# Performance work log

Measured on AMD Instinct MI355X. Metric: run time of the kernel, lower is better.

## Reference

```python
import jax, jax.numpy as jnp
import numpy as np

C = 256
HEADS = 4
GROUPS = 8
EPS = 1e-5


def setup_inputs() -> dict:
    key = jax.random.key(0)
    ks = jax.random.split(key, 7)
    B, H, W = 2, 64, 64
    x = jax.random.normal(ks[0], (B, C, H, W), dtype=jnp.float32)
    gamma = jnp.ones((C,), dtype=jnp.float32)
    beta = jnp.zeros((C,), dtype=jnp.float32)
    # conv 1x1 weights stored as [out_ch, in_ch]
    w_qkv = jax.random.normal(ks[1], (3 * C, C), dtype=jnp.float32) * (1.0 / np.sqrt(C))
    b_qkv = jax.random.normal(ks[2], (3 * C,), dtype=jnp.float32) * 0.01
    w_proj = jax.random.normal(ks[3], (C, C), dtype=jnp.float32) * (1.0 / np.sqrt(C))
    b_proj = jax.random.normal(ks[4], (C,), dtype=jnp.float32) * 0.01
    return {"x": x, "gamma": gamma, "beta": beta, "w_qkv": w_qkv,
            "b_qkv": b_qkv, "w_proj": w_proj, "b_proj": b_proj}


def _group_norm(x, gamma, beta):
    B, Cc, H, W = x.shape
    xg = x.reshape(B, GROUPS, Cc // GROUPS, H, W)
    mean = xg.mean(axis=(2, 3, 4), keepdims=True)
    var = xg.var(axis=(2, 3, 4), keepdims=True)
    xg = (xg - mean) * jax.lax.rsqrt(var + EPS)
    xn = xg.reshape(B, Cc, H, W)
    return xn * gamma[None, :, None, None] + beta[None, :, None, None]


def reference(x, gamma, beta, w_qkv, b_qkv, w_proj, b_proj):
    B, Cc, H, W = x.shape
    N = H * W
    hd = Cc // HEADS
    residual = x
    xn = _group_norm(x, gamma, beta)
    # 1x1 conv == channel matmul: [B,3C,H,W]
    qkv = jnp.einsum('oc,bchw->bohw', w_qkv, xn) + b_qkv[None, :, None, None]
    # [B,3,heads,hd,N] -> (3,B,heads,N,hd)
    qkv = qkv.reshape(B, 3, HEADS, hd, N).transpose(1, 0, 2, 4, 3)
    q, k, v = qkv[0], qkv[1], qkv[2]
    scale = hd ** -0.5
    attn = jax.nn.softmax(jnp.einsum('bhnd,bhmd->bhnm', q, k) * scale, axis=-1)
    out = jnp.einsum('bhnm,bhmd->bhnd', attn, v)  # [B,heads,N,hd]
    out = out.transpose(0, 1, 3, 2).reshape(B, Cc, H, W)
    out = jnp.einsum('oc,bchw->bohw', w_proj, out) + b_proj[None, :, None, None]
    return out + residual
```

## Files before the change

### kernel.cpp

```cpp
#include <hip/hip_runtime.h>
#include <stdint.h>

#define EPS 1e-5f

typedef float f32x4 __attribute__((ext_vector_type(4)));
typedef float f32x16 __attribute__((ext_vector_type(16)));
typedef __bf16 bf16x8 __attribute__((ext_vector_type(8)));
typedef uint32_t u32x4 __attribute__((ext_vector_type(4)));

__device__ __forceinline__ ushort f2bf(float f){
  union { float f; uint32_t u; } v; v.f = f;
  uint32_t r = v.u + 0x7fffu + ((v.u >> 16) & 1u);
  return (ushort)(r >> 16);
}

__device__ __forceinline__ float bf2f(ushort u){
  union { uint32_t u; float f; } v; v.u = ((uint32_t)u) << 16;
  return v.f;
}

__device__ __forceinline__ uint32_t pk2bf(float a, float b){
  __bf16 x = (__bf16)a, y = (__bf16)b;
  return (uint32_t)__builtin_bit_cast(ushort, x) |
         ((uint32_t)__builtin_bit_cast(ushort, y) << 16);
}

__device__ __forceinline__ f32x4 mfma16(bf16x8 a, bf16x8 b, f32x4 c){
  return __builtin_amdgcn_mfma_f32_16x16x32_bf16(a, b, c, 0, 0, 0);
}
__device__ __forceinline__ f32x16 mfma32(bf16x8 a, bf16x8 b, f32x16 c){
  return __builtin_amdgcn_mfma_f32_32x32x16_bf16(a, b, c, 0, 0, 0);
}

__global__ __launch_bounds__(256) void k_pg(const float* wq, const float* wp, const float* x,
                                            ushort* wqb, ushort* wpb, float2* part){
  __shared__ float red[8];
  int bid = blockIdx.x;
  if (bid < 768){
    int i = bid * 256 + threadIdx.x;
    if (i < 3*256*256) wqb[i] = f2bf(wq[i]);
    if (i < 256*256)   wpb[i] = f2bf(wp[i]);
    return;
  }
  int gb = bid - 768;
  int bg = gb >> 6, pb = gb & 63;
  const f32x4* base = (const f32x4*)(x + (size_t)bg*131072 + (size_t)pb*2048);
  float s = 0.f, ss = 0.f;
  #pragma unroll
  for (int it = 0; it < 2; ++it){
    f32x4 v = base[threadIdx.x + it*256];
    #pragma unroll
    for (int j = 0; j < 4; ++j){ s += v[j]; ss += v[j]*v[j]; }
  }
  #pragma unroll
  for (int off = 1; off < 64; off <<= 1){
    s  += __shfl_xor(s,  off);
    ss += __shfl_xor(ss, off);
  }
  int wid = threadIdx.x >> 6;
  if ((threadIdx.x & 63) == 0){ red[wid] = s; red[4 + wid] = ss; }
  __syncthreads();
  if (threadIdx.x == 0){
    part[gb] = make_float2(red[0]+red[1]+red[2]+red[3],
                           red[4]+red[5]+red[6]+red[7]);
  }
}

__global__ __launch_bounds__(512) void k_nqkv(const float* x, const float* gamma, const float* beta,
                                              const float2* part, const ushort* wqb, const float* bqkv,
                                              ushort* Qf, ushort* Kf, ushort* Vf){
  __shared__ ushort A[32][264];
  __shared__ ushort Cl[32][136];
  __shared__ ushort Cl_T[128][40];
  __shared__ float2 st[8];
  int nt = blockIdx.x, b = blockIdx.y;
  int t = threadIdx.x, lane = t & 63, wid = t >> 6;

  {
    float2 p = part[(b*8 + wid)*64 + lane];
    float s = p.x, ss = p.y;
    #pragma unroll
    for (int off = 1; off < 64; off <<= 1){
      s  += __shfl_xor(s,  off);
      ss += __shfl_xor(ss, off);
    }
    if (lane == 0){
      const float inv = 1.f / 131072.f;
      float mean = s * inv;
      float var  = ss * inv - mean*mean;
      st[wid] = make_float2(mean, rsqrtf(var + EPS));
    }
  }
  __syncthreads();

  {
    int c = t >> 1, nh = t & 1;
    float2 s0 = st[c >> 5];
    float g  = gamma[c] * s0.y;
    float bt = beta[c] - s0.x * g;
    const float* xr = x + ((size_t)(b*256 + c))*4096 + nt*32 + nh*16;
    #pragma unroll
    for (int j4 = 0; j4 < 4; ++j4){
      f32x4 v = *(const f32x4*)(xr + j4*4);
      #pragma unroll
      for (int e = 0; e < 4; ++e) A[nh*16 + j4*4 + e][c] = f2bf(v[e]*g + bt);
    }
  }
  __syncthreads();

  int l15 = lane & 15, g4 = lane >> 4;
  f32x4 acc[6][2];
  #pragma unroll
  for (int of = 0; of < 6; ++of)
    #pragma unroll
    for (int mf = 0; mf < 2; ++mf) acc[of][mf] = (f32x4){0.f,0.f,0.f,0.f};

  #pragma unroll
  for (int ks = 0; ks < 8; ++ks){
    bf16x8 a0 = *(const bf16x8*)&A[l15][ks*32 + g4*8];
    bf16x8 a1 = *(const bf16x8*)&A[16 + l15][ks*32 + g4*8];
    #pragma unroll
    for (int of = 0; of < 6; ++of){
      int o = of*128 + wid*16 + l15;
      bf16x8 bw = *(const bf16x8*)(wqb + (size_t)o*256 + ks*32 + g4*8);
      acc[of][0] = mfma16(a0, bw, acc[of][0]);
      acc[of][1] = mfma16(a1, bw, acc[of][1]);
    }
  }

  #pragma unroll
  for (int of = 0; of < 6; ++of){
    __syncthreads();
    float bias = bqkv[of*128 + wid*16 + l15];
    if (of < 4){
      #pragma unroll
      for (int mf = 0; mf < 2; ++mf)
        #pragma unroll
        for (int r = 0; r < 4; ++r)
          Cl[mf*16 + g4*4 + r][wid*16 + l15] = f2bf(acc[of][mf][r] + bias);
    } else {
      #pragma unroll
      for (int mf = 0; mf < 2; ++mf)
        *(uint2*)&Cl_T[wid*16 + l15][mf*16 + g4*4] =
          make_uint2(pk2bf(acc[of][mf][0]+bias, acc[of][mf][1]+bias),
                     pk2bf(acc[of][mf][2]+bias, acc[of][mf][3]+bias));
    }
    __syncthreads();

    int hp = t >> 8;
    int hh = (of & 1)*2 + hp;
    if (of < 4){
      int rem = t & 255, dsub = rem >> 6, ln = rem & 63, h2 = ln >> 5, p31 = ln & 31;
      int row = (of < 2) ? p31 : ((p31 & 19) | ((p31 & 4) << 1) | ((p31 & 8) >> 1));
      ushort* basep = (of < 2) ? Qf : Kf;
      uint4 v = *(const uint4*)&Cl[row][hp*64 + dsub*16 + h2*8];
      *(uint4*)(basep + ((size_t)(b*4 + hh))*262144 + nt*2048 + dsub*512 + ln*8) = v;
    } else {
      int rem = t & 255, dt = rem >> 7, r2 = rem & 127, c4h = r2 >> 5, p31 = r2 & 31;
      int c4 = (nt & 1)*2 + (c4h >> 1), h2 = c4h & 1;
      int n0 = (c4h >> 1)*16 + h2*8;
      int ln = h2*32 + p31;
      uint4 v = *(const uint4*)&Cl_T[hp*64 + dt*32 + p31][n0];
      *(uint4*)(Vf + ((size_t)(b*4 + hh))*262144 + (size_t)(nt >> 1)*4096
                   + dt*2048 + c4*512 + ln*8) = v;
    }
  }
}

template<int SPLIT>
__global__ __launch_bounds__(64, 3) void k_attn(const ushort* Qf, const ushort* Kf,
                                                const ushort* Vf, ushort* Opart, float2* ML){
  const float SCL2 = 0.125f * 1.44269504f;
  int bh = blockIdx.x & 7;
  int within = blockIdx.x >> 3;
  int sp = within >> 7, qt = within & 127;
  int l = threadIdx.x, l31 = l & 31, hi = l >> 5;

  const ushort* Qg = Qf + (size_t)bh*262144 + qt*2048 + l*8;
  const ushort* Kg = Kf + (size_t)bh*262144 + l*8;
  const ushort* Vg = Vf + (size_t)bh*262144 + l*8;

  bf16x8 qf[4];
  #pragma unroll
  for (int dsub = 0; dsub < 4; ++dsub)
    qf[dsub] = *(const bf16x8*)(Qg + dsub*512);

  f32x16 o[2];
  #pragma unroll
  for (int dt = 0; dt < 2; ++dt)
    #pragma unroll
    for (int r = 0; r < 16; ++r) o[dt][r] = 0.f;
  float m_s = -INFINITY, l_s = 0.f;

  const int kbBeg = sp * (64 / SPLIT), kbEnd = kbBeg + 64 / SPLIT;
  for (int kb = kbBeg; kb < kbEnd; ++kb){
    bf16x8 kf[2][4];
    #pragma unroll
    for (int kt = 0; kt < 2; ++kt)
      #pragma unroll
      for (int dsub = 0; dsub < 4; ++dsub)
        kf[kt][dsub] = *(const bf16x8*)(Kg + (size_t)(kb*2 + kt)*2048 + dsub*512);

    bf16x8 vf[2][4];
    #pragma unroll
    for (int dt = 0; dt < 2; ++dt)
      #pragma unroll
      for (int c4 = 0; c4 < 4; ++c4)
        vf[dt][c4] = *(const bf16x8*)(Vg + (size_t)kb*4096 + dt*2048 + c4*512);

    f32x16 s[2];
    __builtin_amdgcn_s_setprio(1);
    #pragma unroll
    for (int kt = 0; kt < 2; ++kt){
      f32x16 acc;
      #pragma unroll
      for (int r = 0; r < 16; ++r) acc[r] = 0.f;
      #pragma unroll
      for (int dsub = 0; dsub < 4; ++dsub)
        acc = mfma32(kf[kt][dsub], qf[dsub], acc);
      s[kt] = acc;
    }
    __builtin_amdgcn_s_setprio(0);

    f32x16 mx = s[0];
    #pragma unroll
    for (int r = 0; r < 16; ++r) mx[r] = fmaxf(mx[r], s[1][r]);
    #pragma unroll
    for (int off = 8; off > 0; off >>= 1)
      #pragma unroll
      for (int r = 0; r < off; ++r) mx[r] = fmaxf(mx[r], mx[r + off]);
    float vm = fmaxf(mx[0], __shfl_xor(mx[0], 32)) * SCL2;

    if (__any(vm > m_s + 8.f)){
      float mn = fmaxf(m_s, vm);
      float a = __builtin_amdgcn_exp2f(m_s - mn);
      m_s = mn; l_s *= a;
      #pragma unroll
      for (int dt = 0; dt < 2; ++dt)
        #pragma unroll
        for (int r = 0; r < 16; ++r) o[dt][r] *= a;
    }
    {
      float r0 = 0.f, r1 = 0.f, r2 = 0.f, r3 = 0.f;
      #pragma unroll
      for (int kt = 0; kt < 2; ++kt)
        #pragma unroll
        for (int r = 0; r < 16; r += 4){
          float e0 = __builtin_amdgcn_exp2f(__builtin_fmaf(s[kt][r+0], SCL2, -m_s));
          float e1 = __builtin_amdgcn_exp2f(__builtin_fmaf(s[kt][r+1], SCL2, -m_s));
          float e2 = __builtin_amdgcn_exp2f(__builtin_fmaf(s[kt][r+2], SCL2, -m_s));
          float e3 = __builtin_amdgcn_exp2f(__builtin_fmaf(s[kt][r+3], SCL2, -m_s));
          s[kt][r+0] = e0; s[kt][r+1] = e1;
          s[kt][r+2] = e2; s[kt][r+3] = e3;
          r0 += e0; r1 += e1; r2 += e2; r3 += e3;
        }
      float rr = (r0 + r1) + (r2 + r3);
      rr += __shfl_xor(rr, 32);
      l_s += rr;
    }

    bf16x8 pf[2][2];
    #pragma unroll
    for (int kt = 0; kt < 2; ++kt)
      #pragma unroll
      for (int ks = 0; ks < 2; ++ks){
        u32x4 w;
        #pragma unroll
        for (int c = 0; c < 4; ++c)
          w[c] = pk2bf(s[kt][8*ks + 2*c], s[kt][8*ks + 2*c + 1]);
        pf[kt][ks] = __builtin_bit_cast(bf16x8, w);
      }

    __builtin_amdgcn_s_setprio(1);
    #pragma unroll
    for (int dt = 0; dt < 2; ++dt)
      #pragma unroll
      for (int kt = 0; kt < 2; ++kt)
        #pragma unroll
        for (int ks = 0; ks < 2; ++ks)
          o[dt] = mfma32(vf[dt][kt*2 + ks], pf[kt][ks], o[dt]);
    __builtin_amdgcn_s_setprio(0);
  }

  int pw = (bh*SPLIT + sp)*128 + qt;
  if (hi == 0) ML[(size_t)pw*32 + l31] = make_float2(m_s, l_s);
  ushort* dst = Opart + (size_t)pw*2048;
  #pragma unroll
  for (int dt = 0; dt < 2; ++dt)
    #pragma unroll
    for (int rq = 0; rq < 4; ++rq){
      int d0 = dt*32 + rq*8 + 4*hi;
      uint2 w = make_uint2(pk2bf(o[dt][rq*4+0], o[dt][rq*4+1]),
                           pk2bf(o[dt][rq*4+2], o[dt][rq*4+3]));
      *(uint2*)(dst + (size_t)l31*64 + d0) = w;
    }
}

template<int SPLIT>
__global__ __launch_bounds__(512) void k_cproj(const ushort* Opart, const float2* ML,
                                               const ushort* wpb, const float* bproj,
                                               const float* x, float* out){
  __shared__ ushort A[64][264];
  int nt = blockIdx.x, b = blockIdx.y;
  int t = threadIdx.x;

  int n_local = t >> 3, d0 = (t & 7) * 8;
  int tile = n_local >> 5, ql = n_local & 31;
  int qt32 = nt*2 + tile;
  #pragma unroll
  for (int h = 0; h < 4; ++h){
    int bh = b*4 + h;
    float2 mls[SPLIT];
    float m = -INFINITY;
    #pragma unroll
    for (int sp = 0; sp < SPLIT; ++sp){
      mls[sp] = ML[((size_t)((bh*SPLIT + sp)*128 + qt32))*32 + ql];
      m = fmaxf(m, mls[sp].x);
    }
    float den = 0.f, w[SPLIT];
    #pragma unroll
    for (int sp = 0; sp < SPLIT; ++sp){
      w[sp] = __builtin_amdgcn_exp2f(mls[sp].x - m);
      den += mls[sp].y * w[sp];
    }
    float inv = 1.f / den;
    float vals[8];
    #pragma unroll
    for (int j = 0; j < 8; ++j) vals[j] = 0.f;
    #pragma unroll
    for (int sp = 0; sp < SPLIT; ++sp){
      const ushort* src = Opart + ((size_t)((bh*SPLIT + sp)*128 + qt32))*2048 + (size_t)ql*64 + d0;
      uint4 a0 = *(const uint4*)src;
      float f = w[sp] * inv;
      #pragma unroll
      for (int j = 0; j < 8; ++j) vals[j] += bf2f(((const ushort*)&a0)[j]) * f;
    }
    uint32_t pk[4];
    #pragma unroll
    for (int j = 0; j < 4; ++j) pk[j] = pk2bf(vals[2*j], vals[2*j+1]);
    *(uint4*)&A[n_local][h*64 + d0] = make_uint4(pk[0], pk[1], pk[2], pk[3]);
  }
  __syncthreads();

  int lane = t & 63, wid = t >> 6, l15 = lane & 15, g4 = lane >> 4;
  f32x4 acc[4][2];
  #pragma unroll
  for (int mf = 0; mf < 4; ++mf)
    #pragma unroll
    for (int of = 0; of < 2; ++of) acc[mf][of] = (f32x4){0.f,0.f,0.f,0.f};

  #pragma unroll
  for (int ks = 0; ks < 8; ++ks){
    bf16x8 aa[4];
    #pragma unroll
    for (int mf = 0; mf < 4; ++mf)
      aa[mf] = *(const bf16x8*)&A[mf*16 + l15][ks*32 + g4*8];
    #pragma unroll
    for (int of = 0; of < 2; ++of){
      int o = of*128 + wid*16 + l15;
      bf16x8 bw = *(const bf16x8*)(wpb + (size_t)o*256 + ks*32 + g4*8);
      #pragma unroll
      for (int mf = 0; mf < 4; ++mf)
        acc[mf][of] = mfma16(aa[mf], bw, acc[mf][of]);
    }
  }

  #pragma unroll
  for (int of = 0; of < 2; ++of){
    int o = of*128 + wid*16 + l15;
    float bias = bproj[o];
    size_t cbase = ((size_t)b*256 + o)*4096;
    #pragma unroll
    for (int mf = 0; mf < 4; ++mf){
      int n0 = nt*64 + mf*16 + g4*4;
      f32x4 res = *(const f32x4*)(x + cbase + n0);
      f32x4 ov;
      #pragma unroll
      for (int r = 0; r < 4; ++r) ov[r] = acc[mf][of][r] + bias + res[r];
      *(f32x4*)(out + cbase + n0) = ov;
    }
  }
}

extern "C" void kernel_launch(void* const* d_in, const int* in_sizes, int n_in,
                              void* d_out, int out_size, void* d_ws, size_t ws_size,
                              hipStream_t stream) {
  const float* x     = (const float*)d_in[0];
  const float* gamma = (const float*)d_in[1];
  const float* beta  = (const float*)d_in[2];
  const float* wqkv  = (const float*)d_in[3];
  const float* bqkv  = (const float*)d_in[4];
  const float* wproj = (const float*)d_in[5];
  const float* bproj = (const float*)d_in[6];
  float* out = (float*)d_out;

  const size_t MiB = 1024*1024;
  char* ws = (char*)d_ws;
  float2* part   = (float2*)(ws + 0);
  ushort* wq_b   = (ushort*)(ws + 16384);
  ushort* wp_b   = (ushort*)(ws + 409600);
  ushort* Qf     = (ushort*)(ws + 1*MiB);
  ushort* Kf     = (ushort*)(ws + 5*MiB);
  ushort* Vf     = (ushort*)(ws + 9*MiB);
  ushort* Opart  = (ushort*)(ws + 13*MiB);

  int split = (ws_size >= 31*MiB) ? 4 : 2;
  float2* ML = (float2*)(ws + (13 + 4*(size_t)split)*MiB);

  k_pg  <<<1792, 256, 0, stream>>>(wqkv, wproj, x, wq_b, wp_b, part);
  k_nqkv<<<dim3(128,2), 512, 0, stream>>>(x, gamma, beta, part, wq_b, bqkv, Qf, Kf, Vf);
  if (split == 4){
    k_attn<4><<<4096, 64, 0, stream>>>(Qf, Kf, Vf, Opart, ML);
    k_cproj<4><<<dim3(64,2), 512, 0, stream>>>(Opart, ML, wp_b, bproj, x, out);
  } else {
    k_attn<2><<<2048, 64, 0, stream>>>(Qf, Kf, Vf, Opart, ML);
    k_cproj<2><<<dim3(64,2), 512, 0, stream>>>(Opart, ML, wp_b, bproj, x, out);
  }
}
```

Baseline: 153.3 us.

## Fold softmax scale into Q, pack four query tiles per attention block, shrink cproj tiles

The softmax scale and log2e factor are now applied to Q when it is written in the QKV kernel, so the attention inner loop drops one FMA per score element. The attention kernel moves from one 64-thread wave per block to four waves per block, each handling its own query tile, which cuts the block count. The projection kernel now uses 256 threads over 32-row tiles with twice as many blocks, aiming for better occupancy across CUs. Rounding scaled Q to bf16 slightly changes numerics, and the 8.0 rescale threshold now applies in the log2 domain.

```diff
diff --git a/kernel.cpp b/kernel.cpp
--- a/kernel.cpp
+++ b/kernel.cpp
@@ -73,6 +73,7 @@
   __shared__ ushort Cl[32][136];
   __shared__ ushort Cl_T[128][40];
   __shared__ float2 st[8];
+  const float SCL2 = 0.125f * 1.44269504f;
   int nt = blockIdx.x, b = blockIdx.y;
   int t = threadIdx.x, lane = t & 63, wid = t >> 6;
 
@@ -133,11 +134,12 @@
     __syncthreads();
     float bias = bqkv[of*128 + wid*16 + l15];
     if (of < 4){
+      float scl = (of < 2) ? SCL2 : 1.f;
       #pragma unroll
       for (int mf = 0; mf < 2; ++mf)
         #pragma unroll
         for (int r = 0; r < 4; ++r)
-          Cl[mf*16 + g4*4 + r][wid*16 + l15] = f2bf(acc[of][mf][r] + bias);
+          Cl[mf*16 + g4*4 + r][wid*16 + l15] = f2bf((acc[of][mf][r] + bias) * scl);
     } else {
       #pragma unroll
       for (int mf = 0; mf < 2; ++mf)
@@ -168,13 +170,13 @@
 }
 
 template<int SPLIT>
-__global__ __launch_bounds__(64, 3) void k_attn(const ushort* Qf, const ushort* Kf,
-                                                const ushort* Vf, ushort* Opart, float2* ML){
-  const float SCL2 = 0.125f * 1.44269504f;
+__global__ __launch_bounds__(256, 3) void k_attn(const ushort* Qf, const ushort* Kf,
+                                                 const ushort* Vf, ushort* Opart, float2* ML){
   int bh = blockIdx.x & 7;
   int within = blockIdx.x >> 3;
-  int sp = within >> 7, qt = within & 127;
-  int l = threadIdx.x, l31 = l & 31, hi = l >> 5;
+  int sp = within >> 5, qg = within & 31;
+  int t = threadIdx.x, wid = t >> 6, l = t & 63, l31 = l & 31, hi = l >> 5;
+  int qt = qg*4 + wid;
 
   const ushort* Qg = Qf + (size_t)bh*262144 + qt*2048 + l*8;
   const ushort* Kg = Kf + (size_t)bh*262144 + l*8;
@@ -229,7 +231,7 @@
     for (int off = 8; off > 0; off >>= 1)
       #pragma unroll
       for (int r = 0; r < off; ++r) mx[r] = fmaxf(mx[r], mx[r + off]);
-    float vm = fmaxf(mx[0], __shfl_xor(mx[0], 32)) * SCL2;
+    float vm = fmaxf(mx[0], __shfl_xor(mx[0], 32));
 
     if (__any(vm > m_s + 8.f)){
       float mn = fmaxf(m_s, vm);
@@ -246,10 +248,10 @@
       for (int kt = 0; kt < 2; ++kt)
         #pragma unroll
         for (int r = 0; r < 16; r += 4){
-          float e0 = __builtin_amdgcn_exp2f(__builtin_fmaf(s[kt][r+0], SCL2, -m_s));
-          float e1 = __builtin_amdgcn_exp2f(__builtin_fmaf(s[kt][r+1], SCL2, -m_s));
-          float e2 = __builtin_amdgcn_exp2f(__builtin_fmaf(s[kt][r+2], SCL2, -m_s));
-          float e3 = __builtin_amdgcn_exp2f(__builtin_fmaf(s[kt][r+3], SCL2, -m_s));
+          float e0 = __builtin_amdgcn_exp2f(s[kt][r+0] - m_s);
+          float e1 = __builtin_amdgcn_exp2f(s[kt][r+1] - m_s);
+          float e2 = __builtin_amdgcn_exp2f(s[kt][r+2] - m_s);
+          float e3 = __builtin_amdgcn_exp2f(s[kt][r+3] - m_s);
           s[kt][r+0] = e0; s[kt][r+1] = e1;
           s[kt][r+2] = e2; s[kt][r+3] = e3;
           r0 += e0; r1 += e1; r2 += e2; r3 += e3;
@@ -297,16 +299,14 @@
 }
 
 template<int SPLIT>
-__global__ __launch_bounds__(512) void k_cproj(const ushort* Opart, const float2* ML,
+__global__ __launch_bounds__(256) void k_cproj(const ushort* Opart, const float2* ML,
                                                const ushort* wpb, const float* bproj,
                                                const float* x, float* out){
-  __shared__ ushort A[64][264];
+  __shared__ ushort A[32][264];
   int nt = blockIdx.x, b = blockIdx.y;
   int t = threadIdx.x;
 
   int n_local = t >> 3, d0 = (t & 7) * 8;
-  int tile = n_local >> 5, ql = n_local & 31;
-  int qt32 = nt*2 + tile;
   #pragma unroll
   for (int h = 0; h < 4; ++h){
     int bh = b*4 + h;
@@ -314,7 +314,7 @@
     float m = -INFINITY;
     #pragma unroll
     for (int sp = 0; sp < SPLIT; ++sp){
-      mls[sp] = ML[((size_t)((bh*SPLIT + sp)*128 + qt32))*32 + ql];
+      mls[sp] = ML[((size_t)((bh*SPLIT + sp)*128 + nt))*32 + n_local];
       m = fmaxf(m, mls[sp].x);
     }
     float den = 0.f, w[SPLIT];
@@ -329,7 +329,7 @@
     for (int j = 0; j < 8; ++j) vals[j] = 0.f;
     #pragma unroll
     for (int sp = 0; sp < SPLIT; ++sp){
-      const ushort* src = Opart + ((size_t)((bh*SPLIT + sp)*128 + qt32))*2048 + (size_t)ql*64 + d0;
+      const ushort* src = Opart + ((size_t)((bh*SPLIT + sp)*128 + nt))*2048 + (size_t)n_local*64 + d0;
       uint4 a0 = *(const uint4*)src;
       float f = w[sp] * inv;
       #pragma unroll
@@ -345,38 +345,35 @@
   int lane = t & 63, wid = t >> 6, l15 = lane & 15, g4 = lane >> 4;
   f32x4 acc[4][2];
   #pragma unroll
-  for (int mf = 0; mf < 4; ++mf)
-    #pragma unroll
-    for (int of = 0; of < 2; ++of) acc[mf][of] = (f32x4){0.f,0.f,0.f,0.f};
+  for (int of = 0; of < 4; ++of)
+    #pragma unroll
+    for (int mf = 0; mf < 2; ++mf) acc[of][mf] = (f32x4){0.f,0.f,0.f,0.f};
 
   #pragma unroll
   for (int ks = 0; ks < 8; ++ks){
-    bf16x8 aa[4];
-    #pragma unroll
-    for (int mf = 0; mf < 4; ++mf)
-      aa[mf] = *(const bf16x8*)&A[mf*16 + l15][ks*32 + g4*8];
-    #pragma unroll
-    for (int of = 0; of < 2; ++of){
-      int o = of*128 + wid*16 + l15;
+    bf16x8 aa0 = *(const bf16x8*)&A[l15][ks*32 + g4*8];
+    bf16x8 aa1 = *(const bf16x8*)&A[16 + l15][ks*32 + g4*8];
+    #pragma unroll
+    for (int of = 0; of < 4; ++of){
+      int o = wid*64 + of*16 + l15;
       bf16x8 bw = *(const bf16x8*)(wpb + (size_t)o*256 + ks*32 + g4*8);
-      #pragma unroll
-      for (int mf = 0; mf < 4; ++mf)
-        acc[mf][of] = mfma16(aa[mf], bw, acc[mf][of]);
-    }
-  }
-
-  #pragma unroll
-  for (int of = 0; of < 2; ++of){
-    int o = of*128 + wid*16 + l15;
+      acc[of][0] = mfma16(aa0, bw, acc[of][0]);
+      acc[of][1] = mfma16(aa1, bw, acc[of][1]);
+    }
+  }
+
+  #pragma unroll
+  for (int of = 0; of < 4; ++of){
+    int o = wid*64 + of*16 + l15;
     float bias = bproj[o];
     size_t cbase = ((size_t)b*256 + o)*4096;
     #pragma unroll
-    for (int mf = 0; mf < 4; ++mf){
-      int n0 = nt*64 + mf*16 + g4*4;
+    for (int mf = 0; mf < 2; ++mf){
+      int n0 = nt*32 + mf*16 + g4*4;
       f32x4 res = *(const f32x4*)(x + cbase + n0);
       f32x4 ov;
       #pragma unroll
-      for (int r = 0; r < 4; ++r) ov[r] = acc[mf][of][r] + bias + res[r];
+      for (int r = 0; r < 4; ++r) ov[r] = acc[of][mf][r] + bias + res[r];
       *(f32x4*)(out + cbase + n0) = ov;
     }
   }
@@ -410,10 +407,10 @@
   k_pg  <<<1792, 256, 0, stream>>>(wqkv, wproj, x, wq_b, wp_b, part);
   k_nqkv<<<dim3(128,2), 512, 0, stream>>>(x, gamma, beta, part, wq_b, bqkv, Qf, Kf, Vf);
   if (split == 4){
-    k_attn<4><<<4096, 64, 0, stream>>>(Qf, Kf, Vf, Opart, ML);
-    k_cproj<4><<<dim3(64,2), 512, 0, stream>>>(Opart, ML, wp_b, bproj, x, out);
+    k_attn<4><<<1024, 256, 0, stream>>>(Qf, Kf, Vf, Opart, ML);
+    k_cproj<4><<<dim3(128,2), 256, 0, stream>>>(Opart, ML, wp_b, bproj, x, out);
   } else {
-    k_attn<2><<<2048, 64, 0, stream>>>(Qf, Kf, Vf, Opart, ML);
-    k_cproj<2><<<dim3(64,2), 512, 0, stream>>>(Opart, ML, wp_b, bproj, x, out);
-  }
-}
+    k_attn<2><<<512, 256, 0, stream>>>(Qf, Kf, Vf, Opart, ML);
+    k_cproj<2><<<dim3(128,2), 256, 0, stream>>>(Opart, ML, wp_b, bproj, x, out);
+  }
+}
```

New measurement: 154.4 us. Within noise of the previous version (+0.7%).
